# Optimization experiments

Hardware: AMD Instinct MI355X
Metric: run time of the kernel (lower is better)

The kernel has to match this reference:

```python
import jax, jax.numpy as jnp
from jax import lax
import numpy as np


def setup_inputs() -> dict:
    key = jax.random.key(0)
    ks = jax.random.split(key, 9)
    B, T_enc, D = 32, 2048, 512   # batch, encoder length, enc_dim == nb_dims
    T_dec, U = 128, 512           # decode steps, LSTM units (== out_dim)
    s = 0.05
    return {
        "enc_output": jax.random.normal(ks[0], (B, T_enc, D), jnp.float32),
        "dec_input": jax.random.normal(ks[1], (B, T_dec, U), jnp.float32),
        "W1": jax.random.normal(ks[2], (D, D), jnp.float32) * s,
        "W2": jax.random.normal(ks[3], (U, D), jnp.float32) * s,
        "b2": jnp.zeros((D,), jnp.float32),
        "V": jax.random.normal(ks[4], (D,), jnp.float32) * s,
        "W3": jax.random.normal(ks[5], (D + U, U), jnp.float32) * s,
        "b3": jnp.zeros((U,), jnp.float32),
        "lstm_kernel": jax.random.normal(ks[6], (U, 4 * U), jnp.float32) * s,
        "lstm_rec_kernel": jax.random.normal(ks[7], (U, 4 * U), jnp.float32) * s,
        "lstm_bias": jnp.zeros((4 * U,), jnp.float32),
    }


def reference(enc_output, dec_input, W1, W2, b2, V, W3, b3,
              lstm_kernel, lstm_rec_kernel, lstm_bias):
    # Precomputed constant, as in get_constants(): xW1 = enc_output @ W1
    xW1 = jnp.einsum('bte,ed->btd', enc_output, W1)  # [B, T_enc, D]

    def step(carry, x_t):
        h, c = carry                                  # [B, U] each
        # Bahdanau additive attention score over encoder positions
        hW2 = h @ W2 + b2                             # [B, D]
        u = jnp.tanh(xW1 + hW2[:, None, :])           # [B, T_enc, D]
        scores = jnp.einsum('btd,d->bt', u, V)        # [B, T_enc]
        a = jax.nn.softmax(scores, axis=1)            # [B, T_enc]
        Xa = jnp.einsum('bt,bte->be', a, enc_output)  # [B, D]
        # Mix decoder input with context, then LSTM cell step
        h_in = jnp.concatenate([x_t, Xa], axis=1) @ W3 + b3  # [B, U]
        z = h_in @ lstm_kernel + h @ lstm_rec_kernel + lstm_bias
        zi, zf, zg, zo = jnp.split(z, 4, axis=1)
        i = jax.nn.sigmoid(zi)
        f = jax.nn.sigmoid(zf)
        g = jnp.tanh(zg)
        o = jax.nn.sigmoid(zo)
        c_new = f * c + i * g
        h_new = o * jnp.tanh(c_new)
        return (h_new, c_new), h_new

    B = enc_output.shape[0]
    U = W3.shape[1]
    h0 = jnp.zeros((B, U), enc_output.dtype)
    c0 = jnp.zeros((B, U), enc_output.dtype)
    xs = jnp.swapaxes(dec_input, 0, 1)                # [T_dec, B, U]
    _, ys = lax.scan(step, (h0, c0), xs)              # ys: [T_dec, B, U]
    return jnp.swapaxes(ys, 0, 1)                     # [B, T_dec, U]
```

## Files before the change

### kernel.cpp

```cpp
#include <hip/hip_runtime.h>
#include <cstddef>
#include <cstdint>

#define B 32
#define TENC 2048
#define DD 512
#define TDEC 128
#define UU 512
#define NCH 16
#define TCH 128

typedef unsigned short ushort_t;

__device__ __forceinline__ uint16_t f2bf(float x) {
    uint32_t u = __float_as_uint(x);
    u += 0x7fffu + ((u >> 16) & 1u);
    return (uint16_t)(u >> 16);
}
__device__ __forceinline__ void unpack8(uint4 v, float* f) {
    f[0] = __uint_as_float(v.x << 16); f[1] = __uint_as_float(v.x & 0xffff0000u);
    f[2] = __uint_as_float(v.y << 16); f[3] = __uint_as_float(v.y & 0xffff0000u);
    f[4] = __uint_as_float(v.z << 16); f[5] = __uint_as_float(v.z & 0xffff0000u);
    f[6] = __uint_as_float(v.w << 16); f[7] = __uint_as_float(v.w & 0xffff0000u);
}
__device__ __forceinline__ float fast_tanh(float x) {
    float e = __expf(2.f * x);
    return 1.f - 2.f * __builtin_amdgcn_rcpf(e + 1.f);
}
__device__ __forceinline__ float fast_sig(float x) {
    return __builtin_amdgcn_rcpf(1.f + __expf(-x));
}

__global__ void cvt_kernel(const float* __restrict__ in, ushort_t* __restrict__ out) {
    int i = blockIdx.x * 256 + threadIdx.x;
    const float4* ip = (const float4*)in;
    float4 a = ip[2 * i], b = ip[2 * i + 1];
    uint4 o;
    o.x = (uint32_t)f2bf(a.x) | ((uint32_t)f2bf(a.y) << 16);
    o.y = (uint32_t)f2bf(a.z) | ((uint32_t)f2bf(a.w) << 16);
    o.z = (uint32_t)f2bf(b.x) | ((uint32_t)f2bf(b.y) << 16);
    o.w = (uint32_t)f2bf(b.z) | ((uint32_t)f2bf(b.w) << 16);
    ((uint4*)out)[i] = o;
}

__global__ void gemm_xw1_kernel(const float* __restrict__ A, const float* __restrict__ Bm,
                                ushort_t* __restrict__ C) {
    __shared__ float As[16][65];
    __shared__ float Bs[16][65];
    int bm = blockIdx.y * 64, bn = blockIdx.x * 64;
    int tx = threadIdx.x & 15, ty = threadIdx.x >> 4;
    float acc[4][4] = {};
    for (int k0 = 0; k0 < 512; k0 += 16) {
#pragma unroll
        for (int i = 0; i < 4; i++) {
            int idx = threadIdx.x + 256 * i;
            int r = idx >> 4, kk = idx & 15;
            As[kk][r] = A[(size_t)(bm + r) * 512 + k0 + kk];
            int cc = idx & 63, kb = idx >> 6;
            Bs[kb][cc] = Bm[(size_t)(k0 + kb) * 512 + bn + cc];
        }
        __syncthreads();
#pragma unroll
        for (int kk = 0; kk < 16; kk++) {
            float a[4], b[4];
#pragma unroll
            for (int i = 0; i < 4; i++) a[i] = As[kk][ty * 4 + i];
#pragma unroll
            for (int j = 0; j < 4; j++) b[j] = Bs[kk][tx * 4 + j];
#pragma unroll
            for (int i = 0; i < 4; i++)
#pragma unroll
                for (int j = 0; j < 4; j++) acc[i][j] += a[i] * b[j];
        }
        __syncthreads();
    }
#pragma unroll
    for (int i = 0; i < 4; i++) {
        uint2 o;
        o.x = (uint32_t)f2bf(acc[i][0]) | ((uint32_t)f2bf(acc[i][1]) << 16);
        o.y = (uint32_t)f2bf(acc[i][2]) | ((uint32_t)f2bf(acc[i][3]) << 16);
        *(uint2*)(C + (size_t)(bm + ty * 4 + i) * 512 + bn + tx * 4) = o;
    }
}

__global__ void hw2_kernel(const float* __restrict__ h, const float* __restrict__ W2,
                           const float* __restrict__ b2, float* __restrict__ hW2) {
    int b = blockIdx.x;
    int d = blockIdx.y * 256 + threadIdx.x;
    __shared__ float hs[512];
    hs[threadIdx.x] = h[b * 512 + threadIdx.x];
    hs[threadIdx.x + 256] = h[b * 512 + threadIdx.x + 256];
    __syncthreads();
    float acc = b2[d];
#pragma unroll 8
    for (int u = 0; u < 512; u++) acc += hs[u] * W2[(size_t)u * 512 + d];
    hW2[b * 512 + d] = acc;
}

__global__ void attn_kernel(const ushort_t* __restrict__ xW1h, const ushort_t* __restrict__ ench,
                            const float* __restrict__ hW2, const float* __restrict__ Vv,
                            float* __restrict__ pm, float* __restrict__ pl,
                            float* __restrict__ pacc) {
    int b = blockIdx.x, ch = blockIdx.y;
    int tid = threadIdx.x, wave = tid >> 6, lane = tid & 63;

    float hs[8], vs[8];
    {
        const float4* hp = (const float4*)(hW2 + b * 512 + lane * 8);
        float4 h0 = hp[0], h1 = hp[1];
        hs[0] = h0.x; hs[1] = h0.y; hs[2] = h0.z; hs[3] = h0.w;
        hs[4] = h1.x; hs[5] = h1.y; hs[6] = h1.z; hs[7] = h1.w;
        const float4* vp = (const float4*)(Vv + lane * 8);
        float4 v0 = vp[0], v1 = vp[1];
        vs[0] = v0.x; vs[1] = v0.y; vs[2] = v0.z; vs[3] = v0.w;
        vs[4] = v1.x; vs[5] = v1.y; vs[6] = v1.z; vs[7] = v1.w;
    }

    int t0 = ch * TCH + wave * 32;
    const uint4* xr = (const uint4*)xW1h + ((size_t)b * TENC + t0) * 64 + lane;
    const uint4* er = (const uint4*)ench + ((size_t)b * TENC + t0) * 64 + lane;

    float m = -INFINITY, l = 0.f;
    float acc[8] = {0.f, 0.f, 0.f, 0.f, 0.f, 0.f, 0.f, 0.f};

#pragma unroll 2
    for (int tt = 0; tt < 32; ++tt) {
        uint4 xv = xr[tt * 64];
        uint4 ev = er[tt * 64];
        float xf[8], ef[8];
        unpack8(xv, xf);
        float s = 0.f;
#pragma unroll
        for (int j = 0; j < 8; j++) s += fast_tanh(xf[j] + hs[j]) * vs[j];
#pragma unroll
        for (int off = 32; off >= 1; off >>= 1) s += __shfl_xor(s, off, 64);
        float mn = fmaxf(m, s);
        float scale = __expf(m - mn);
        float p = __expf(s - mn);
        l = l * scale + p;
        unpack8(ev, ef);
#pragma unroll
        for (int j = 0; j < 8; j++) acc[j] = acc[j] * scale + p * ef[j];
        m = mn;
    }

    __shared__ float sm[4], sl[4];
    __shared__ float sacc[4][512];
    if (lane == 0) { sm[wave] = m; sl[wave] = l; }
    __syncthreads();
    float bm = fmaxf(fmaxf(sm[0], sm[1]), fmaxf(sm[2], sm[3]));
    float f = __expf(m - bm);
#pragma unroll
    for (int j = 0; j < 8; j++) sacc[wave][lane * 8 + j] = acc[j] * f;
    __syncthreads();
    float s0 = sacc[0][tid] + sacc[1][tid] + sacc[2][tid] + sacc[3][tid];
    float s1 = sacc[0][tid + 256] + sacc[1][tid + 256] + sacc[2][tid + 256] + sacc[3][tid + 256];
    size_t po = ((size_t)(b * NCH + ch)) * 512;
    pacc[po + tid] = s0;
    pacc[po + tid + 256] = s1;
    if (tid == 0) {
        pm[b * NCH + ch] = bm;
        pl[b * NCH + ch] = sl[0] * __expf(sm[0] - bm) + sl[1] * __expf(sm[1] - bm) +
                           sl[2] * __expf(sm[2] - bm) + sl[3] * __expf(sm[3] - bm);
    }
}

__global__ void combine_kernel(const float* __restrict__ pm, const float* __restrict__ pl,
                               const float* __restrict__ pacc, float* __restrict__ Xa) {
    int b = blockIdx.x, tid = threadIdx.x;
    __shared__ float w[NCH];
    float mg = -1e30f;
#pragma unroll
    for (int i = 0; i < NCH; i++) mg = fmaxf(mg, pm[b * NCH + i]);
    float L = 0.f;
#pragma unroll
    for (int i = 0; i < NCH; i++) L += pl[b * NCH + i] * __expf(pm[b * NCH + i] - mg);
    if (tid < NCH) w[tid] = __expf(pm[b * NCH + tid] - mg);
    __syncthreads();
    float inv = __builtin_amdgcn_rcpf(L);
    for (int d = tid; d < 512; d += 256) {
        float s = 0.f;
#pragma unroll
        for (int i = 0; i < NCH; i++) s += w[i] * pacc[((size_t)(b * NCH + i)) * 512 + d];
        Xa[b * 512 + d] = s * inv;
    }
}

__global__ void mix_kernel(const float* __restrict__ dec, const float* __restrict__ Xa,
                           const float* __restrict__ W3, const float* __restrict__ b3,
                           float* __restrict__ h_in, int t) {
    int u0 = blockIdx.x * 16;
    int tx = threadIdx.x & 15, ty = threadIdx.x >> 4;
    __shared__ float s[32][65];
    __shared__ float Ws[64][17];
    float acc0 = 0.f, acc1 = 0.f;
    for (int k0 = 0; k0 < 1024; k0 += 64) {
#pragma unroll
        for (int i = 0; i < 8; i++) {
            int idx = threadIdx.x + 256 * i;
            int bb = idx >> 6, kk = idx & 63;
            int k = k0 + kk;
            s[bb][kk] = (k < 512) ? dec[((size_t)bb * TDEC + t) * 512 + k]
                                  : Xa[bb * 512 + (k - 512)];
        }
#pragma unroll
        for (int i = 0; i < 4; i++) {
            int idx = threadIdx.x + 256 * i;
            int kk = idx >> 4, uu = idx & 15;
            Ws[kk][uu] = W3[(size_t)(k0 + kk) * 512 + u0 + uu];
        }
        __syncthreads();
#pragma unroll
        for (int k = 0; k < 64; k++) {
            float w = Ws[k][tx];
            acc0 += s[ty][k] * w;
            acc1 += s[ty + 16][k] * w;
        }
        __syncthreads();
    }
    float bv = b3[u0 + tx];
    h_in[ty * 512 + u0 + tx] = acc0 + bv;
    h_in[(ty + 16) * 512 + u0 + tx] = acc1 + bv;
}

__global__ void z_kernel(const float* __restrict__ h_in, const float* __restrict__ h,
                         const float* __restrict__ Wk, const float* __restrict__ Wr,
                         const float* __restrict__ bias, float* __restrict__ z) {
    int gc = blockIdx.x * 16;
    int tx = threadIdx.x & 15, ty = threadIdx.x >> 4;
    __shared__ float his[32][65], hcs[32][65], Ks[64][16], Rs[64][16];
    float acc0 = 0.f, acc1 = 0.f;
    for (int u0 = 0; u0 < 512; u0 += 64) {
#pragma unroll
        for (int i = 0; i < 8; i++) {
            int idx = threadIdx.x + 256 * i;
            int bb = idx >> 6, uu = idx & 63;
            his[bb][uu] = h_in[bb * 512 + u0 + uu];
            hcs[bb][uu] = h[bb * 512 + u0 + uu];
        }
#pragma unroll
        for (int i = 0; i < 4; i++) {
            int idx = threadIdx.x + 256 * i;
            int uu = idx >> 4, gg = idx & 15;
            Ks[uu][gg] = Wk[(size_t)(u0 + uu) * 2048 + gc + gg];
            Rs[uu][gg] = Wr[(size_t)(u0 + uu) * 2048 + gc + gg];
        }
        __syncthreads();
#pragma unroll
        for (int u = 0; u < 64; u++) {
            float kv = Ks[u][tx], rv = Rs[u][tx];
            acc0 += his[ty][u] * kv + hcs[ty][u] * rv;
            acc1 += his[ty + 16][u] * kv + hcs[ty + 16][u] * rv;
        }
        __syncthreads();
    }
    float bv = bias[gc + tx];
    z[(size_t)ty * 2048 + gc + tx] = acc0 + bv;
    z[(size_t)(ty + 16) * 2048 + gc + tx] = acc1 + bv;
}

__global__ void gate_kernel(const float* __restrict__ z, float* __restrict__ c,
                            float* __restrict__ h, float* __restrict__ out, int t) {
    int idx = blockIdx.x * 256 + threadIdx.x;
    int b = idx >> 9, u = idx & 511;
    const float* zb = z + (size_t)b * 2048;
    float zi = zb[u], zf = zb[512 + u], zg = zb[1024 + u], zo = zb[1536 + u];
    float ig = fast_sig(zi);
    float fg = fast_sig(zf);
    float gg = fast_tanh(zg);
    float og = fast_sig(zo);
    float cn = fg * c[idx] + ig * gg;
    float hn = og * fast_tanh(cn);
    c[idx] = cn;
    h[idx] = hn;
    out[((size_t)b * TDEC + t) * 512 + u] = hn;
}

extern "C" void kernel_launch(void* const* d_in, const int* in_sizes, int n_in,
                              void* d_out, int out_size, void* d_ws, size_t ws_size,
                              hipStream_t stream) {
    const float* enc = (const float*)d_in[0];
    const float* dec = (const float*)d_in[1];
    const float* W1 = (const float*)d_in[2];
    const float* W2 = (const float*)d_in[3];
    const float* b2 = (const float*)d_in[4];
    const float* V = (const float*)d_in[5];
    const float* W3 = (const float*)d_in[6];
    const float* b3 = (const float*)d_in[7];
    const float* Wk = (const float*)d_in[8];
    const float* Wr = (const float*)d_in[9];
    const float* bias = (const float*)d_in[10];
    float* out = (float*)d_out;

    char* ws = (char*)d_ws;
    size_t o = 0;
    ushort_t* xW1h = (ushort_t*)(ws + o); o += (size_t)B * TENC * 512 * 2;
    ushort_t* ench = (ushort_t*)(ws + o); o += (size_t)B * TENC * 512 * 2;
    float* pacc = (float*)(ws + o); o += (size_t)B * NCH * 512 * 4;
    float* h = (float*)(ws + o);    o += B * 512 * 4;
    float* c = (float*)(ws + o);    o += B * 512 * 4;
    float* hW2 = (float*)(ws + o);  o += B * 512 * 4;
    float* Xa = (float*)(ws + o);   o += B * 512 * 4;
    float* h_in = (float*)(ws + o); o += B * 512 * 4;
    float* z = (float*)(ws + o);    o += B * 2048 * 4;
    float* pm = (float*)(ws + o);   o += B * NCH * 4;
    float* pl = (float*)(ws + o);   o += B * NCH * 4;

    hipMemsetAsync(h, 0, (size_t)2 * B * 512 * sizeof(float), stream);

    cvt_kernel<<<16384, 256, 0, stream>>>(enc, ench);
    gemm_xw1_kernel<<<dim3(8, 1024), 256, 0, stream>>>(enc, W1, xW1h);

    for (int t = 0; t < TDEC; t++) {
        hw2_kernel<<<dim3(32, 2), 256, 0, stream>>>(h, W2, b2, hW2);
        attn_kernel<<<dim3(32, NCH), 256, 0, stream>>>(xW1h, ench, hW2, V, pm, pl, pacc);
        combine_kernel<<<32, 256, 0, stream>>>(pm, pl, pacc, Xa);
        mix_kernel<<<32, 256, 0, stream>>>(dec, Xa, W3, b3, h_in, t);
        z_kernel<<<128, 256, 0, stream>>>(h_in, h, Wk, Wr, bias, z);
        gate_kernel<<<64, 256, 0, stream>>>(z, c, h, out, t);
    }
}
```

Before: 21.10 ms.

## Fuse decode loop into one cooperative persistent kernel with precomputed MFMA GEMMs

Replaces the six per-step kernel launches with one cooperative persistent kernel that loops over all decode steps and separates phases with grid syncs. The input projection path (dec@W3a@Wk) is hoisted out of the loop as batched bf16 MFMA GEMMs, and W3b@Wk is folded into a single context-to-gate matrix, which also drops the h_in intermediate. The xW1 GEMM moves to MFMA with transposed bf16 weights, and the attention chunk count is halved. This targets launch overhead and per-step small-GEMM cost, at the price of grid-wide barriers and extra bf16 rounding in the precomputed products.

Result: slower. 22.91 ms (+8.6%).

```diff
diff --git a/kernel.cpp b/kernel.cpp
--- a/kernel.cpp
+++ b/kernel.cpp
@@ -1,21 +1,27 @@
 #include <hip/hip_runtime.h>
+#include <hip/hip_cooperative_groups.h>
 #include <cstddef>
 #include <cstdint>
 
+namespace cg = cooperative_groups;
+
 #define B 32
 #define TENC 2048
-#define DD 512
 #define TDEC 128
-#define UU 512
-#define NCH 16
-#define TCH 128
+#define NCH 8
+#define TCH 256
 
 typedef unsigned short ushort_t;
+typedef __attribute__((ext_vector_type(8))) short short8;
+typedef __attribute__((ext_vector_type(4))) float floatx4;
 
 __device__ __forceinline__ uint16_t f2bf(float x) {
     uint32_t u = __float_as_uint(x);
     u += 0x7fffu + ((u >> 16) & 1u);
     return (uint16_t)(u >> 16);
+}
+__device__ __forceinline__ float bf2f(ushort_t u) {
+    return __uint_as_float(((uint32_t)u) << 16);
 }
 __device__ __forceinline__ void unpack8(uint4 v, float* f) {
     f[0] = __uint_as_float(v.x << 16); f[1] = __uint_as_float(v.x & 0xffff0000u);
@@ -43,237 +49,273 @@
     ((uint4*)out)[i] = o;
 }
 
-__global__ void gemm_xw1_kernel(const float* __restrict__ A, const float* __restrict__ Bm,
-                                ushort_t* __restrict__ C) {
-    __shared__ float As[16][65];
-    __shared__ float Bs[16][65];
-    int bm = blockIdx.y * 64, bn = blockIdx.x * 64;
-    int tx = threadIdx.x & 15, ty = threadIdx.x >> 4;
-    float acc[4][4] = {};
-    for (int k0 = 0; k0 < 512; k0 += 16) {
-#pragma unroll
-        for (int i = 0; i < 4; i++) {
-            int idx = threadIdx.x + 256 * i;
-            int r = idx >> 4, kk = idx & 15;
-            As[kk][r] = A[(size_t)(bm + r) * 512 + k0 + kk];
-            int cc = idx & 63, kb = idx >> 6;
-            Bs[kb][cc] = Bm[(size_t)(k0 + kb) * 512 + bn + cc];
-        }
-        __syncthreads();
-#pragma unroll
-        for (int kk = 0; kk < 16; kk++) {
-            float a[4], b[4];
-#pragma unroll
-            for (int i = 0; i < 4; i++) a[i] = As[kk][ty * 4 + i];
-#pragma unroll
-            for (int j = 0; j < 4; j++) b[j] = Bs[kk][tx * 4 + j];
-#pragma unroll
-            for (int i = 0; i < 4; i++)
-#pragma unroll
-                for (int j = 0; j < 4; j++) acc[i][j] += a[i] * b[j];
-        }
-        __syncthreads();
-    }
+__global__ void tr_cvt_bf16_kernel(const float* __restrict__ in, ushort_t* __restrict__ out,
+                                   int R, int C) {
+    __shared__ float tile[32][33];
+    int r0 = blockIdx.y * 32, c0 = blockIdx.x * 32;
+    int tx = threadIdx.x & 31, ty = threadIdx.x >> 5;
 #pragma unroll
     for (int i = 0; i < 4; i++) {
-        uint2 o;
-        o.x = (uint32_t)f2bf(acc[i][0]) | ((uint32_t)f2bf(acc[i][1]) << 16);
-        o.y = (uint32_t)f2bf(acc[i][2]) | ((uint32_t)f2bf(acc[i][3]) << 16);
-        *(uint2*)(C + (size_t)(bm + ty * 4 + i) * 512 + bn + tx * 4) = o;
-    }
-}
-
-__global__ void hw2_kernel(const float* __restrict__ h, const float* __restrict__ W2,
-                           const float* __restrict__ b2, float* __restrict__ hW2) {
-    int b = blockIdx.x;
-    int d = blockIdx.y * 256 + threadIdx.x;
-    __shared__ float hs[512];
-    hs[threadIdx.x] = h[b * 512 + threadIdx.x];
-    hs[threadIdx.x + 256] = h[b * 512 + threadIdx.x + 256];
+        int r = ty + i * 8;
+        tile[r][tx] = in[(size_t)(r0 + r) * C + c0 + tx];
+    }
     __syncthreads();
-    float acc = b2[d];
+#pragma unroll
+    for (int i = 0; i < 4; i++) {
+        int rr = ty + i * 8;
+        out[(size_t)(c0 + rr) * R + r0 + tx] = f2bf(tile[tx][rr]);
+    }
+}
+__global__ void tr_f32_kernel(const float* __restrict__ in, float* __restrict__ out,
+                              int R, int C) {
+    __shared__ float tile[32][33];
+    int r0 = blockIdx.y * 32, c0 = blockIdx.x * 32;
+    int tx = threadIdx.x & 31, ty = threadIdx.x >> 5;
+#pragma unroll
+    for (int i = 0; i < 4; i++) {
+        int r = ty + i * 8;
+        tile[r][tx] = in[(size_t)(r0 + r) * C + c0 + tx];
+    }
+    __syncthreads();
+#pragma unroll
+    for (int i = 0; i < 4; i++) {
+        int rr = ty + i * 8;
+        out[(size_t)(c0 + rr) * R + r0 + tx] = tile[tx][rr];
+    }
+}
+
+__global__ void bz_kernel(const float* __restrict__ b3, const float* __restrict__ Wk,
+                          const float* __restrict__ bias, float* __restrict__ bz) {
+    int g = blockIdx.x * 256 + threadIdx.x;
+    float s = bias[g];
 #pragma unroll 8
-    for (int u = 0; u < 512; u++) acc += hs[u] * W2[(size_t)u * 512 + d];
-    hW2[b * 512 + d] = acc;
-}
-
-__global__ void attn_kernel(const ushort_t* __restrict__ xW1h, const ushort_t* __restrict__ ench,
-                            const float* __restrict__ hW2, const float* __restrict__ Vv,
-                            float* __restrict__ pm, float* __restrict__ pl,
-                            float* __restrict__ pacc) {
-    int b = blockIdx.x, ch = blockIdx.y;
+    for (int u = 0; u < 512; u++) s += b3[u] * Wk[(size_t)u * 2048 + g];
+    bz[g] = s;
+}
+
+template <int BF16OUT>
+__global__ void mfma_gemm_kernel(const ushort_t* __restrict__ A, const ushort_t* __restrict__ Bt,
+                                 void* __restrict__ C, int M, int N) {
     int tid = threadIdx.x, wave = tid >> 6, lane = tid & 63;
-
-    float hs[8], vs[8];
-    {
-        const float4* hp = (const float4*)(hW2 + b * 512 + lane * 8);
-        float4 h0 = hp[0], h1 = hp[1];
-        hs[0] = h0.x; hs[1] = h0.y; hs[2] = h0.z; hs[3] = h0.w;
-        hs[4] = h1.x; hs[5] = h1.y; hs[6] = h1.z; hs[7] = h1.w;
-        const float4* vp = (const float4*)(Vv + lane * 8);
-        float4 v0 = vp[0], v1 = vp[1];
-        vs[0] = v0.x; vs[1] = v0.y; vs[2] = v0.z; vs[3] = v0.w;
-        vs[4] = v1.x; vs[5] = v1.y; vs[6] = v1.z; vs[7] = v1.w;
-    }
-
-    int t0 = ch * TCH + wave * 32;
-    const uint4* xr = (const uint4*)xW1h + ((size_t)b * TENC + t0) * 64 + lane;
-    const uint4* er = (const uint4*)ench + ((size_t)b * TENC + t0) * 64 + lane;
-
-    float m = -INFINITY, l = 0.f;
-    float acc[8] = {0.f, 0.f, 0.f, 0.f, 0.f, 0.f, 0.f, 0.f};
-
+    int wy = wave & 1, wx = wave >> 1;
+    int m0 = blockIdx.y * 64 + wy * 32;
+    int n0 = blockIdx.x * 64 + wx * 32;
+    int lr = lane & 15, quad = lane >> 4;
+    floatx4 a00 = {0.f, 0.f, 0.f, 0.f}, a01 = a00, a10 = a00, a11 = a00;
+    const short8* Ap0 = (const short8*)(A + (size_t)(m0 + lr) * 512 + quad * 8);
+    const short8* Ap1 = (const short8*)(A + (size_t)(m0 + 16 + lr) * 512 + quad * 8);
+    const short8* Bp0 = (const short8*)(Bt + (size_t)(n0 + lr) * 512 + quad * 8);
+    const short8* Bp1 = (const short8*)(Bt + (size_t)(n0 + 16 + lr) * 512 + quad * 8);
+#pragma unroll 4
+    for (int k = 0; k < 16; k++) {
+        short8 av0 = Ap0[k * 4], av1 = Ap1[k * 4];
+        short8 bv0 = Bp0[k * 4], bv1 = Bp1[k * 4];
+        a00 = __builtin_amdgcn_mfma_f32_16x16x32_bf16(av0, bv0, a00, 0, 0, 0);
+        a01 = __builtin_amdgcn_mfma_f32_16x16x32_bf16(av0, bv1, a01, 0, 0, 0);
+        a10 = __builtin_amdgcn_mfma_f32_16x16x32_bf16(av1, bv0, a10, 0, 0, 0);
+        a11 = __builtin_amdgcn_mfma_f32_16x16x32_bf16(av1, bv1, a11, 0, 0, 0);
+    }
+    int rb = quad * 4;
+    if (BF16OUT) {
+        ushort_t* Cp = (ushort_t*)C;
+#pragma unroll
+        for (int r = 0; r < 4; r++) {
+            Cp[(size_t)(m0 + rb + r) * N + n0 + lr] = f2bf(a00[r]);
+            Cp[(size_t)(m0 + rb + r) * N + n0 + 16 + lr] = f2bf(a01[r]);
+            Cp[(size_t)(m0 + 16 + rb + r) * N + n0 + lr] = f2bf(a10[r]);
+            Cp[(size_t)(m0 + 16 + rb + r) * N + n0 + 16 + lr] = f2bf(a11[r]);
+        }
+    } else {
+        float* Cp = (float*)C;
+#pragma unroll
+        for (int r = 0; r < 4; r++) {
+            Cp[(size_t)(m0 + rb + r) * N + n0 + lr] = a00[r];
+            Cp[(size_t)(m0 + rb + r) * N + n0 + 16 + lr] = a01[r];
+            Cp[(size_t)(m0 + 16 + rb + r) * N + n0 + lr] = a10[r];
+            Cp[(size_t)(m0 + 16 + rb + r) * N + n0 + 16 + lr] = a11[r];
+        }
+    }
+}
+
+__global__ __launch_bounds__(256, 1) void step_kernel(
+    const ushort_t* __restrict__ xW1h, const ushort_t* __restrict__ ench,
+    const ushort_t* __restrict__ Zxh, const float* __restrict__ bz,
+    const float* __restrict__ W2t, const float* __restrict__ Wrt,
+    const float* __restrict__ Wazt, const float* __restrict__ Vv,
+    const float* __restrict__ b2,
+    float* __restrict__ h, float* __restrict__ c, float* __restrict__ hW2,
+    float* __restrict__ zbuf, float* __restrict__ pm, float* __restrict__ pl,
+    float* __restrict__ pacc, float* __restrict__ Xa, float* __restrict__ out) {
+    cg::grid_group grid = cg::this_grid();
+    int bk = blockIdx.x, tid = threadIdx.x;
+    int wave = tid >> 6, lane = tid & 63;
+    __shared__ float smem[21560];
+
+    for (int t = 0; t < TDEC; ++t) {
+        {
+            for (int idx = tid; idx < 16384; idx += 256)
+                smem[(idx >> 9) * 513 + (idx & 511)] = h[idx];
+            int n0 = bk * 10;
+            for (int idx = tid; idx < 5120; idx += 256) {
+                int cc = idx >> 9, d = idx & 511;
+                int n = n0 + cc;
+                const float* src = (n < 512) ? (W2t + (size_t)n * 512)
+                                             : (Wrt + (size_t)(n - 512) * 512);
+                smem[16416 + cc * 513 + d] = src[d];
+            }
+            __syncthreads();
+            int q = tid & 3;
+#pragma unroll
+            for (int r = 0; r < 5; ++r) {
+                int o = r * 64 + (tid >> 2);
+                int cc = o >> 5, b = o & 31;
+                const float* hrow = smem + b * 513;
+                const float* wrow = smem + 16416 + cc * 513;
+                float acc = 0.f;
+#pragma unroll 8
+                for (int i = 0; i < 128; ++i) {
+                    int d = q + 4 * i;
+                    acc += hrow[d] * wrow[d];
+                }
+                acc += __shfl_xor(acc, 1, 64);
+                acc += __shfl_xor(acc, 2, 64);
+                if (q == 0) {
+                    int n = n0 + cc;
+                    if (n < 512) {
+                        hW2[b * 512 + n] = acc + b2[n];
+                    } else {
+                        int g = n - 512;
+                        float zx = bf2f(Zxh[((size_t)(b * 128 + t)) * 2048 + g]);
+                        zbuf[b * 2048 + g] = acc + zx + bz[g];
+                    }
+                }
+            }
+        }
+        grid.sync();
+        {
+            int b = bk >> 3, ch = bk & 7;
+            float hs[8], vs[8];
+            {
+                const float4* hp = (const float4*)(hW2 + b * 512 + lane * 8);
+                float4 h0 = hp[0], h1 = hp[1];
+                hs[0] = h0.x; hs[1] = h0.y; hs[2] = h0.z; hs[3] = h0.w;
+                hs[4] = h1.x; hs[5] = h1.y; hs[6] = h1.z; hs[7] = h1.w;
+                const float4* vp = (const float4*)(Vv + lane * 8);
+                float4 v0 = vp[0], v1 = vp[1];
+                vs[0] = v0.x; vs[1] = v0.y; vs[2] = v0.z; vs[3] = v0.w;
+                vs[4] = v1.x; vs[5] = v1.y; vs[6] = v1.z; vs[7] = v1.w;
+            }
+            int t0 = ch * TCH + wave * 64;
+            const uint4* xr = (const uint4*)xW1h + ((size_t)b * TENC + t0) * 64 + lane;
+            const uint4* er = (const uint4*)ench + ((size_t)b * TENC + t0) * 64 + lane;
+            float m = -INFINITY, l = 0.f;
+            float acc[8] = {0.f, 0.f, 0.f, 0.f, 0.f, 0.f, 0.f, 0.f};
 #pragma unroll 2
-    for (int tt = 0; tt < 32; ++tt) {
-        uint4 xv = xr[tt * 64];
-        uint4 ev = er[tt * 64];
-        float xf[8], ef[8];
-        unpack8(xv, xf);
-        float s = 0.f;
-#pragma unroll
-        for (int j = 0; j < 8; j++) s += fast_tanh(xf[j] + hs[j]) * vs[j];
-#pragma unroll
-        for (int off = 32; off >= 1; off >>= 1) s += __shfl_xor(s, off, 64);
-        float mn = fmaxf(m, s);
-        float scale = __expf(m - mn);
-        float p = __expf(s - mn);
-        l = l * scale + p;
-        unpack8(ev, ef);
-#pragma unroll
-        for (int j = 0; j < 8; j++) acc[j] = acc[j] * scale + p * ef[j];
-        m = mn;
-    }
-
-    __shared__ float sm[4], sl[4];
-    __shared__ float sacc[4][512];
-    if (lane == 0) { sm[wave] = m; sl[wave] = l; }
-    __syncthreads();
-    float bm = fmaxf(fmaxf(sm[0], sm[1]), fmaxf(sm[2], sm[3]));
-    float f = __expf(m - bm);
-#pragma unroll
-    for (int j = 0; j < 8; j++) sacc[wave][lane * 8 + j] = acc[j] * f;
-    __syncthreads();
-    float s0 = sacc[0][tid] + sacc[1][tid] + sacc[2][tid] + sacc[3][tid];
-    float s1 = sacc[0][tid + 256] + sacc[1][tid + 256] + sacc[2][tid + 256] + sacc[3][tid + 256];
-    size_t po = ((size_t)(b * NCH + ch)) * 512;
-    pacc[po + tid] = s0;
-    pacc[po + tid + 256] = s1;
-    if (tid == 0) {
-        pm[b * NCH + ch] = bm;
-        pl[b * NCH + ch] = sl[0] * __expf(sm[0] - bm) + sl[1] * __expf(sm[1] - bm) +
-                           sl[2] * __expf(sm[2] - bm) + sl[3] * __expf(sm[3] - bm);
-    }
-}
-
-__global__ void combine_kernel(const float* __restrict__ pm, const float* __restrict__ pl,
-                               const float* __restrict__ pacc, float* __restrict__ Xa) {
-    int b = blockIdx.x, tid = threadIdx.x;
-    __shared__ float w[NCH];
-    float mg = -1e30f;
-#pragma unroll
-    for (int i = 0; i < NCH; i++) mg = fmaxf(mg, pm[b * NCH + i]);
-    float L = 0.f;
-#pragma unroll
-    for (int i = 0; i < NCH; i++) L += pl[b * NCH + i] * __expf(pm[b * NCH + i] - mg);
-    if (tid < NCH) w[tid] = __expf(pm[b * NCH + tid] - mg);
-    __syncthreads();
-    float inv = __builtin_amdgcn_rcpf(L);
-    for (int d = tid; d < 512; d += 256) {
-        float s = 0.f;
-#pragma unroll
-        for (int i = 0; i < NCH; i++) s += w[i] * pacc[((size_t)(b * NCH + i)) * 512 + d];
-        Xa[b * 512 + d] = s * inv;
-    }
-}
-
-__global__ void mix_kernel(const float* __restrict__ dec, const float* __restrict__ Xa,
-                           const float* __restrict__ W3, const float* __restrict__ b3,
-                           float* __restrict__ h_in, int t) {
-    int u0 = blockIdx.x * 16;
-    int tx = threadIdx.x & 15, ty = threadIdx.x >> 4;
-    __shared__ float s[32][65];
-    __shared__ float Ws[64][17];
-    float acc0 = 0.f, acc1 = 0.f;
-    for (int k0 = 0; k0 < 1024; k0 += 64) {
-#pragma unroll
-        for (int i = 0; i < 8; i++) {
-            int idx = threadIdx.x + 256 * i;
-            int bb = idx >> 6, kk = idx & 63;
-            int k = k0 + kk;
-            s[bb][kk] = (k < 512) ? dec[((size_t)bb * TDEC + t) * 512 + k]
-                                  : Xa[bb * 512 + (k - 512)];
-        }
-#pragma unroll
-        for (int i = 0; i < 4; i++) {
-            int idx = threadIdx.x + 256 * i;
-            int kk = idx >> 4, uu = idx & 15;
-            Ws[kk][uu] = W3[(size_t)(k0 + kk) * 512 + u0 + uu];
-        }
-        __syncthreads();
-#pragma unroll
-        for (int k = 0; k < 64; k++) {
-            float w = Ws[k][tx];
-            acc0 += s[ty][k] * w;
-            acc1 += s[ty + 16][k] * w;
-        }
-        __syncthreads();
-    }
-    float bv = b3[u0 + tx];
-    h_in[ty * 512 + u0 + tx] = acc0 + bv;
-    h_in[(ty + 16) * 512 + u0 + tx] = acc1 + bv;
-}
-
-__global__ void z_kernel(const float* __restrict__ h_in, const float* __restrict__ h,
-                         const float* __restrict__ Wk, const float* __restrict__ Wr,
-                         const float* __restrict__ bias, float* __restrict__ z) {
-    int gc = blockIdx.x * 16;
-    int tx = threadIdx.x & 15, ty = threadIdx.x >> 4;
-    __shared__ float his[32][65], hcs[32][65], Ks[64][16], Rs[64][16];
-    float acc0 = 0.f, acc1 = 0.f;
-    for (int u0 = 0; u0 < 512; u0 += 64) {
-#pragma unroll
-        for (int i = 0; i < 8; i++) {
-            int idx = threadIdx.x + 256 * i;
-            int bb = idx >> 6, uu = idx & 63;
-            his[bb][uu] = h_in[bb * 512 + u0 + uu];
-            hcs[bb][uu] = h[bb * 512 + u0 + uu];
-        }
-#pragma unroll
-        for (int i = 0; i < 4; i++) {
-            int idx = threadIdx.x + 256 * i;
-            int uu = idx >> 4, gg = idx & 15;
-            Ks[uu][gg] = Wk[(size_t)(u0 + uu) * 2048 + gc + gg];
-            Rs[uu][gg] = Wr[(size_t)(u0 + uu) * 2048 + gc + gg];
-        }
-        __syncthreads();
-#pragma unroll
-        for (int u = 0; u < 64; u++) {
-            float kv = Ks[u][tx], rv = Rs[u][tx];
-            acc0 += his[ty][u] * kv + hcs[ty][u] * rv;
-            acc1 += his[ty + 16][u] * kv + hcs[ty + 16][u] * rv;
-        }
-        __syncthreads();
-    }
-    float bv = bias[gc + tx];
-    z[(size_t)ty * 2048 + gc + tx] = acc0 + bv;
-    z[(size_t)(ty + 16) * 2048 + gc + tx] = acc1 + bv;
-}
-
-__global__ void gate_kernel(const float* __restrict__ z, float* __restrict__ c,
-                            float* __restrict__ h, float* __restrict__ out, int t) {
-    int idx = blockIdx.x * 256 + threadIdx.x;
-    int b = idx >> 9, u = idx & 511;
-    const float* zb = z + (size_t)b * 2048;
-    float zi = zb[u], zf = zb[512 + u], zg = zb[1024 + u], zo = zb[1536 + u];
-    float ig = fast_sig(zi);
-    float fg = fast_sig(zf);
-    float gg = fast_tanh(zg);
-    float og = fast_sig(zo);
-    float cn = fg * c[idx] + ig * gg;
-    float hn = og * fast_tanh(cn);
-    c[idx] = cn;
-    h[idx] = hn;
-    out[((size_t)b * TDEC + t) * 512 + u] = hn;
+            for (int tt = 0; tt < 64; ++tt) {
+                uint4 xv = xr[(size_t)tt * 64];
+                uint4 ev = er[(size_t)tt * 64];
+                float xf[8], ef[8];
+                unpack8(xv, xf);
+                float s = 0.f;
+#pragma unroll
+                for (int j = 0; j < 8; j++) s += fast_tanh(xf[j] + hs[j]) * vs[j];
+#pragma unroll
+                for (int off = 32; off >= 1; off >>= 1) s += __shfl_xor(s, off, 64);
+                float mn = fmaxf(m, s);
+                float sc = __expf(m - mn);
+                float p = __expf(s - mn);
+                l = l * sc + p;
+                unpack8(ev, ef);
+#pragma unroll
+                for (int j = 0; j < 8; j++) acc[j] = acc[j] * sc + p * ef[j];
+                m = mn;
+            }
+            float* smv = smem;
+            float* slv = smem + 8;
+            float* sacc = smem + 16;
+            if (lane == 0) { smv[wave] = m; slv[wave] = l; }
+            __syncthreads();
+            float bmx = fmaxf(fmaxf(smv[0], smv[1]), fmaxf(smv[2], smv[3]));
+            float f = __expf(m - bmx);
+#pragma unroll
+            for (int j = 0; j < 8; j++) sacc[wave * 512 + lane * 8 + j] = acc[j] * f;
+            __syncthreads();
+            float s0 = sacc[tid] + sacc[512 + tid] + sacc[1024 + tid] + sacc[1536 + tid];
+            float s1 = sacc[tid + 256] + sacc[512 + tid + 256] + sacc[1024 + tid + 256] +
+                       sacc[1536 + tid + 256];
+            size_t po = ((size_t)(b * NCH + ch)) * 512;
+            pacc[po + tid] = s0;
+            pacc[po + tid + 256] = s1;
+            if (tid == 0) {
+                pm[b * NCH + ch] = bmx;
+                pl[b * NCH + ch] = slv[0] * __expf(smv[0] - bmx) + slv[1] * __expf(smv[1] - bmx) +
+                                   slv[2] * __expf(smv[2] - bmx) + slv[3] * __expf(smv[3] - bmx);
+            }
+        }
+        grid.sync();
+        {
+            int b = bk >> 3, ds0 = (bk & 7) * 64;
+            if (tid < 64) {
+                float mg = -1e30f;
+#pragma unroll
+                for (int i = 0; i < NCH; i++) mg = fmaxf(mg, pm[b * NCH + i]);
+                float w[NCH];
+                float L = 0.f;
+#pragma unroll
+                for (int i = 0; i < NCH; i++) {
+                    w[i] = __expf(pm[b * NCH + i] - mg);
+                    L += pl[b * NCH + i] * w[i];
+                }
+                float inv = __builtin_amdgcn_rcpf(L);
+                int d = ds0 + tid;
+                float s = 0.f;
+#pragma unroll
+                for (int i = 0; i < NCH; i++)
+                    s += w[i] * pacc[((size_t)(b * NCH + i)) * 512 + d];
+                Xa[b * 512 + d] = s * inv;
+            }
+        }
+        grid.sync();
+        {
+            for (int idx = tid; idx < 16384; idx += 256)
+                smem[(idx >> 9) * 513 + (idx & 511)] = Xa[idx];
+            int u0 = bk * 2;
+            for (int idx = tid; idx < 4096; idx += 256) {
+                int rw = idx >> 9, d = idx & 511;
+                int g = (rw >> 1) * 512 + u0 + (rw & 1);
+                smem[16416 + rw * 513 + d] = Wazt[(size_t)g * 512 + d];
+            }
+            __syncthreads();
+            int col = tid >> 5, b = tid & 31;
+            const float* xrow = smem + b * 513;
+            const float* wrow = smem + 16416 + col * 513;
+            float acc = 0.f;
+#pragma unroll 8
+            for (int d = 0; d < 512; ++d) acc += xrow[d] * wrow[d];
+            int g = (col >> 1) * 512 + u0 + (col & 1);
+            smem[20800 + col * 32 + b] = acc + zbuf[b * 2048 + g];
+            __syncthreads();
+            if (tid < 64) {
+                int bb = tid >> 1, uo = tid & 1;
+                int u = u0 + uo;
+                float zi = smem[20800 + (0 + uo) * 32 + bb];
+                float zf = smem[20800 + (2 + uo) * 32 + bb];
+                float zg = smem[20800 + (4 + uo) * 32 + bb];
+                float zo = smem[20800 + (6 + uo) * 32 + bb];
+                float ig = fast_sig(zi);
+                float fg = fast_sig(zf);
+                float gg = fast_tanh(zg);
+                float og = fast_sig(zo);
+                int idx = bb * 512 + u;
+                float cn = fg * c[idx] + ig * gg;
+                float hn = og * fast_tanh(cn);
+                c[idx] = cn;
+                h[idx] = hn;
+                out[((size_t)bb * TDEC + t) * 512 + u] = hn;
+            }
+        }
+        grid.sync();
+    }
 }
 
 extern "C" void kernel_launch(void* const* d_in, const int* in_sizes, int n_in,
@@ -294,29 +336,50 @@
 
     char* ws = (char*)d_ws;
     size_t o = 0;
-    ushort_t* xW1h = (ushort_t*)(ws + o); o += (size_t)B * TENC * 512 * 2;
-    ushort_t* ench = (ushort_t*)(ws + o); o += (size_t)B * TENC * 512 * 2;
-    float* pacc = (float*)(ws + o); o += (size_t)B * NCH * 512 * 4;
-    float* h = (float*)(ws + o);    o += B * 512 * 4;
-    float* c = (float*)(ws + o);    o += B * 512 * 4;
-    float* hW2 = (float*)(ws + o);  o += B * 512 * 4;
-    float* Xa = (float*)(ws + o);   o += B * 512 * 4;
-    float* h_in = (float*)(ws + o); o += B * 512 * 4;
-    float* z = (float*)(ws + o);    o += B * 2048 * 4;
-    float* pm = (float*)(ws + o);   o += B * NCH * 4;
-    float* pl = (float*)(ws + o);   o += B * NCH * 4;
-
-    hipMemsetAsync(h, 0, (size_t)2 * B * 512 * sizeof(float), stream);
+    auto alloc = [&](size_t bytes) {
+        void* p = ws + o;
+        o += (bytes + 255) & ~(size_t)255;
+        return p;
+    };
+    ushort_t* xW1h = (ushort_t*)alloc(67108864);
+    ushort_t* ench = (ushort_t*)alloc(67108864);
+    ushort_t* Zxh = (ushort_t*)alloc(16777216);
+    ushort_t* dech = (ushort_t*)alloc(4194304);
+    ushort_t* T1h = (ushort_t*)alloc(4194304);
+    ushort_t* W1t = (ushort_t*)alloc(524288);
+    ushort_t* W3h = (ushort_t*)alloc(1048576);
+    ushort_t* W3at = (ushort_t*)alloc(524288);
+    ushort_t* Wkt = (ushort_t*)alloc(2097152);
+    float* W2t = (float*)alloc(1048576);
+    float* Wrt = (float*)alloc(4194304);
+    float* Wazt = (float*)alloc(4194304);
+    float* bz = (float*)alloc(8192);
+    float* h = (float*)alloc(65536);
+    float* c = (float*)alloc(65536);
+    float* hW2 = (float*)alloc(65536);
+    float* Xa = (float*)alloc(65536);
+    float* zbuf = (float*)alloc(262144);
+    float* pm = (float*)alloc(1024);
+    float* pl = (float*)alloc(1024);
+    float* pacc = (float*)alloc(524288);
+
+    hipMemsetAsync(h, 0, 131072, stream);
 
     cvt_kernel<<<16384, 256, 0, stream>>>(enc, ench);
-    gemm_xw1_kernel<<<dim3(8, 1024), 256, 0, stream>>>(enc, W1, xW1h);
-
-    for (int t = 0; t < TDEC; t++) {
-        hw2_kernel<<<dim3(32, 2), 256, 0, stream>>>(h, W2, b2, hW2);
-        attn_kernel<<<dim3(32, NCH), 256, 0, stream>>>(xW1h, ench, hW2, V, pm, pl, pacc);
-        combine_kernel<<<32, 256, 0, stream>>>(pm, pl, pacc, Xa);
-        mix_kernel<<<32, 256, 0, stream>>>(dec, Xa, W3, b3, h_in, t);
-        z_kernel<<<128, 256, 0, stream>>>(h_in, h, Wk, Wr, bias, z);
-        gate_kernel<<<64, 256, 0, stream>>>(z, c, h, out, t);
-    }
-}
+    cvt_kernel<<<1024, 256, 0, stream>>>(dec, dech);
+    cvt_kernel<<<256, 256, 0, stream>>>(W3, W3h);
+    tr_cvt_bf16_kernel<<<dim3(16, 16), 256, 0, stream>>>(W1, W1t, 512, 512);
+    tr_cvt_bf16_kernel<<<dim3(16, 16), 256, 0, stream>>>(W3, W3at, 512, 512);
+    tr_cvt_bf16_kernel<<<dim3(64, 16), 256, 0, stream>>>(Wk, Wkt, 512, 2048);
+    tr_f32_kernel<<<dim3(16, 16), 256, 0, stream>>>(W2, W2t, 512, 512);
+    tr_f32_kernel<<<dim3(64, 16), 256, 0, stream>>>(Wr, Wrt, 512, 2048);
+    bz_kernel<<<8, 256, 0, stream>>>(b3, Wk, bias, bz);
+    mfma_gemm_kernel<1><<<dim3(8, 1024), 256, 0, stream>>>(ench, W1t, xW1h, 65536, 512);
+    mfma_gemm_kernel<1><<<dim3(8, 64), 256, 0, stream>>>(dech, W3at, T1h, 4096, 512);
+    mfma_gemm_kernel<1><<<dim3(32, 64), 256, 0, stream>>>(T1h, Wkt, Zxh, 4096, 2048);
+    mfma_gemm_kernel<0><<<dim3(8, 32), 256, 0, stream>>>(Wkt, W3h + 512 * 512, Wazt, 2048, 512);
+
+    void* args[] = {&xW1h, &ench, &Zxh, &bz, &W2t, &Wrt, &Wazt, &V, &b2,
+                    &h, &c, &hW2, &zbuf, &pm, &pl, &pacc, &Xa, &out};
+    hipLaunchCooperativeKernel((void*)step_kernel, dim3(256), dim3(256), args, 0, stream);
+}
```
